# Kernel optimization log

Measured on AMD Instinct MI355X. Metric: run time of the kernel, lower is better.

Reference implementation:

```python
import jax, jax.numpy as jnp
import numpy as np
from jax import lax

VOCAB, EMBED, HIDDEN, SEQ = 50257, 1024, 1024, 4096


def setup_inputs() -> dict:
    key = jax.random.key(0)
    ks = jax.random.split(key, 8)
    s = 0.02
    return {
        "input_seq": jax.random.randint(ks[0], (SEQ,), 0, VOCAB),
        "emb": jax.random.normal(ks[1], (VOCAB, EMBED), jnp.float32) * s,
        "Wrx": jax.random.normal(ks[2], (HIDDEN, EMBED), jnp.float32) * s,
        "Wrh": jax.random.normal(ks[3], (HIDDEN, HIDDEN), jnp.float32) * s,
        "Wzx": jax.random.normal(ks[4], (HIDDEN, EMBED), jnp.float32) * s,
        "Wzh": jax.random.normal(ks[5], (HIDDEN, HIDDEN), jnp.float32) * s,
        "Wx": jax.random.normal(ks[6], (HIDDEN, EMBED), jnp.float32) * s,
        "Wh": jax.random.normal(ks[7], (HIDDEN, HIDDEN), jnp.float32) * s,
    }


def reference(input_seq, emb, Wrx, Wrh, Wzx, Wzh, Wx, Wh):
    # Embed whole sequence at once: [S, E]
    x_seq = emb[input_seq]
    # Hoist input-side projections out of the recurrence (one GEMM each): [S, H]
    xr = x_seq @ Wrx.T
    xz = x_seq @ Wzx.T
    xh = x_seq @ Wx.T

    def step(h, xs):
        xr_t, xz_t, xh_t = xs
        z = jax.nn.sigmoid(xz_t + Wzh @ h)          # update gate
        r = jax.nn.sigmoid(xr_t + Wrh @ h)          # reset gate
        h_tilde = jnp.tanh(xh_t + Wh @ (r * h))     # candidate
        h_new = z * h + (1.0 - z) * h_tilde
        return h_new, None

    h0 = jnp.zeros((Wh.shape[0],), dtype=emb.dtype)
    h_final, _ = lax.scan(step, h0, (xr, xz, xh))
    return h_final
```

## Files before the change

kernel.cpp:

```cpp
#include <hip/hip_runtime.h>
#include <stdint.h>


#define HID    1024
#define SEQLEN 4096
#define NWG    64
#define RPW    16
#define BLOCK  512

typedef unsigned long long u64;

__global__ __launch_bounds__(256) void proj_gemm(
    const int* __restrict__ seq, const float* __restrict__ emb,
    const float* __restrict__ Wrx, const float* __restrict__ Wzx,
    const float* __restrict__ Wx,
    float* __restrict__ xrT, float* __restrict__ xzT, float* __restrict__ xhT)
{
  __shared__ float As[32][68];
  __shared__ float Bs[32][68];
  __shared__ int   idx[64];

  const float* W = (blockIdx.z == 0) ? Wrx : (blockIdx.z == 1) ? Wzx : Wx;
  float*       C = (blockIdx.z == 0) ? xrT : (blockIdx.z == 1) ? xzT : xhT;

  const int tid = threadIdx.x;
  const int t0 = blockIdx.y * 64;
  const int i0 = blockIdx.x * 64;
  if (tid < 64) idx[tid] = seq[t0 + tid];
  __syncthreads();

  float acc[4][4] = {};
  const int tx = tid & 15, ty = tid >> 4;
  const int c4 = (tid & 7) * 4;
  const int r8 = tid >> 3;

  for (int k0 = 0; k0 < HID; k0 += 32) {
    for (int l = 0; l < 2; ++l) {
      const int rr = r8 + l * 32;
      float4 av = *(const float4*)(emb + (size_t)idx[rr] * HID + k0 + c4);
      As[c4+0][rr]=av.x; As[c4+1][rr]=av.y; As[c4+2][rr]=av.z; As[c4+3][rr]=av.w;
      float4 bv = *(const float4*)(W + (size_t)(i0 + rr) * HID + k0 + c4);
      Bs[c4+0][rr]=bv.x; Bs[c4+1][rr]=bv.y; Bs[c4+2][rr]=bv.z; Bs[c4+3][rr]=bv.w;
    }
    __syncthreads();
    #pragma unroll
    for (int k = 0; k < 32; ++k) {
      float a[4], b[4];
      *(float4*)a = *(const float4*)&Bs[k][ty * 4];
      *(float4*)b = *(const float4*)&As[k][tx * 4];
      #pragma unroll
      for (int i = 0; i < 4; ++i)
        #pragma unroll
        for (int j = 0; j < 4; ++j)
          acc[i][j] = fmaf(a[i], b[j], acc[i][j]);
    }
    __syncthreads();
  }
  #pragma unroll
  for (int i = 0; i < 4; ++i) {
    float4 v = make_float4(acc[i][0], acc[i][1], acc[i][2], acc[i][3]);
    *(float4*)(C + (size_t)(i0 + ty * 4 + i) * SEQLEN + t0 + tx * 4) = v;
  }
}

__device__ __forceinline__ void publish2(u64* cells, int row, float a, float b,
                                         unsigned tag) {
  u64 ca = ((u64)tag << 32) | (u64)__float_as_uint(a);
  u64 cb = ((u64)tag << 32) | (u64)__float_as_uint(b);
  (void)__hip_atomic_exchange(&cells[row],     ca, __ATOMIC_RELAXED,
                              __HIP_MEMORY_SCOPE_AGENT);
  (void)__hip_atomic_exchange(&cells[row + 1], cb, __ATOMIC_RELAXED,
                              __HIP_MEMORY_SCOPE_AGENT);
}

__device__ __forceinline__ float2 poll_pair(const u64* cells, int pair,
                                            unsigned want, int* budget) {
  const u64* p = cells + 2 * pair;
  u64 c0, c1;
  for (;;) {
    c0 = __hip_atomic_load((u64*)(p + 0), __ATOMIC_RELAXED,
                           __HIP_MEMORY_SCOPE_AGENT);
    c1 = __hip_atomic_load((u64*)(p + 1), __ATOMIC_RELAXED,
                           __HIP_MEMORY_SCOPE_AGENT);
    if ((unsigned)(c0 >> 32) == want && (unsigned)(c1 >> 32) == want) break;
    if (--(*budget) <= 0) break;
  }
  return make_float2(__uint_as_float((unsigned)c0),
                     __uint_as_float((unsigned)c1));
}

__global__ __launch_bounds__(BLOCK, 2) void rnn_scan(
    const float* __restrict__ Wzh, const float* __restrict__ Wrh,
    const float* __restrict__ Whh,
    const float* __restrict__ xzT, const float* __restrict__ xrT,
    const float* __restrict__ xhT,
    u64* __restrict__ hcell,
    u64* __restrict__ rhcell,
    float* __restrict__ out)
{
  const int tid  = threadIdx.x;
  const int wave = tid >> 6, lane = tid & 63;
  const int g    = blockIdx.x;
  const int rowA = g * RPW + wave * 2;

  __shared__ float h_lds[HID];
  __shared__ float rh_lds[HID];

  float wgt[3][2][16];
  #pragma unroll
  for (int m = 0; m < 3; ++m) {
    const float* Wm = (m == 0) ? Wzh : (m == 1) ? Wrh : Whh;
    #pragma unroll
    for (int rr = 0; rr < 2; ++rr) {
      const float* p = Wm + (size_t)(rowA + rr) * HID + lane * 4;
      #pragma unroll
      for (int q = 0; q < 4; ++q) {
        float4 v = *(const float4*)(p + q * 256);
        wgt[m][rr][q*4+0] = v.x; wgt[m][rr][q*4+1] = v.y;
        wgt[m][rr][q*4+2] = v.z; wgt[m][rr][q*4+3] = v.w;
      }
    }
  }

  int budget = 1 << 21;
  float xzv[2], xrv[2], xhv[2], zv[2], hprev[2];

  for (int t = 1; t <= SEQLEN; ++t) {
    if (t == 1) {
      *(float2*)&h_lds[2 * tid] = make_float2(0.f, 0.f);
    } else {
      float2 hv = poll_pair(hcell + ((t - 1) & 1) * HID, tid,
                            (unsigned)(t - 1), &budget);
      *(float2*)&h_lds[2 * tid] = hv;
    }

    if (lane == 0) {
      #pragma unroll
      for (int rr = 0; rr < 2; ++rr) {
        xzv[rr] = xzT[(size_t)(rowA + rr) * SEQLEN + (t - 1)];
        xrv[rr] = xrT[(size_t)(rowA + rr) * SEQLEN + (t - 1)];
        xhv[rr] = xhT[(size_t)(rowA + rr) * SEQLEN + (t - 1)];
      }
    }
    __syncthreads();

    float hr[16];
    #pragma unroll
    for (int q = 0; q < 4; ++q)
      *(float4*)&hr[q*4] = *(const float4*)&h_lds[q * 256 + lane * 4];
    float az[2] = {0.f, 0.f}, ar[2] = {0.f, 0.f};
    #pragma unroll
    for (int rr = 0; rr < 2; ++rr)
      #pragma unroll
      for (int c = 0; c < 16; ++c) {
        az[rr] = fmaf(wgt[0][rr][c], hr[c], az[rr]);
        ar[rr] = fmaf(wgt[1][rr][c], hr[c], ar[rr]);
      }
    #pragma unroll
    for (int m = 1; m < 64; m <<= 1) {
      az[0] += __shfl_xor(az[0], m, 64);
      az[1] += __shfl_xor(az[1], m, 64);
      ar[0] += __shfl_xor(ar[0], m, 64);
      ar[1] += __shfl_xor(ar[1], m, 64);
    }
    if (lane == 0) {
      float rh[2];
      #pragma unroll
      for (int rr = 0; rr < 2; ++rr) {
        hprev[rr] = h_lds[rowA + rr];
        zv[rr]    = 1.f / (1.f + __expf(-(xzv[rr] + az[rr])));
        float rg  = 1.f / (1.f + __expf(-(xrv[rr] + ar[rr])));
        rh[rr]    = rg * hprev[rr];
      }
      publish2(rhcell + (t & 1) * HID, rowA, rh[0], rh[1], (unsigned)t);
    }

    {
      float2 rv = poll_pair(rhcell + (t & 1) * HID, tid, (unsigned)t, &budget);
      *(float2*)&rh_lds[2 * tid] = rv;
    }
    __syncthreads();

    float rr16[16];
    #pragma unroll
    for (int q = 0; q < 4; ++q)
      *(float4*)&rr16[q*4] = *(const float4*)&rh_lds[q * 256 + lane * 4];
    float ac[2] = {0.f, 0.f};
    #pragma unroll
    for (int rr = 0; rr < 2; ++rr)
      #pragma unroll
      for (int c = 0; c < 16; ++c)
        ac[rr] = fmaf(wgt[2][rr][c], rr16[c], ac[rr]);
    #pragma unroll
    for (int m = 1; m < 64; m <<= 1) {
      ac[0] += __shfl_xor(ac[0], m, 64);
      ac[1] += __shfl_xor(ac[1], m, 64);
    }
    if (lane == 0) {
      float hn[2];
      #pragma unroll
      for (int rr = 0; rr < 2; ++rr) {
        float cand = tanhf(xhv[rr] + ac[rr]);
        hn[rr]     = zv[rr] * hprev[rr] + (1.f - zv[rr]) * cand;
      }
      publish2(hcell + (t & 1) * HID, rowA, hn[0], hn[1], (unsigned)t);
      if (t == SEQLEN) { out[rowA] = hn[0]; out[rowA + 1] = hn[1]; }
    }
  }
}

extern "C" void kernel_launch(void* const* d_in, const int* in_sizes, int n_in,
                              void* d_out, int out_size, void* d_ws, size_t ws_size,
                              hipStream_t stream) {
  (void)in_sizes; (void)n_in; (void)out_size; (void)ws_size;

  const int*   seq = (const int*)d_in[0];
  const float* emb = (const float*)d_in[1];
  const float* Wrx = (const float*)d_in[2];
  const float* Wrh = (const float*)d_in[3];
  const float* Wzx = (const float*)d_in[4];
  const float* Wzh = (const float*)d_in[5];
  const float* Wx  = (const float*)d_in[6];
  const float* Wh  = (const float*)d_in[7];

  char* ws = (char*)d_ws;
  const size_t PROJ = (size_t)SEQLEN * HID * sizeof(float);
  float* xrT    = (float*)(ws);
  float* xzT    = (float*)(ws + PROJ);
  float* xhT    = (float*)(ws + 2 * PROJ);
  u64*   hcell  = (u64*)(ws + 3 * PROJ);
  u64*   rhcell = hcell + 2 * HID;

  (void)hipMemsetAsync(hcell, 0xFF, 4 * HID * sizeof(u64), stream);

  proj_gemm<<<dim3(HID / 64, SEQLEN / 64, 3), 256, 0, stream>>>(
      seq, emb, Wrx, Wzx, Wx, xrT, xzT, xhT);

  rnn_scan<<<dim3(NWG), BLOCK, 0, stream>>>(
      Wzh, Wrh, Wh, xzT, xrT, xhT, hcell, rhcell, (float*)d_out);
}
```

Measured before the change: 29.70 ms.

## Add spinning filler blocks and busy-FMA warm polling with single wide cache-bypassing load

The recurrent scan kernel is launched with extra blocks that do nothing useful. They spin on dummy FMA chains until the real blocks set a done flag, presumably to keep the device clocked up or resident during the latency-bound scan. The poll loop now also runs dummy FMA work between polls. It reads each tag/value pair with one global_load_dwordx4 carrying sc0 sc1 instead of two 64-bit atomic loads, cutting per-poll load count. The risks are that filler blocks share CUs with real blocks and compete for issue slots and power budget, and that the non-atomic wide load could observe torn tag/value halves.

```diff
diff --git a/kernel.cpp b/kernel.cpp
--- a/kernel.cpp
+++ b/kernel.cpp
@@ -5,6 +5,7 @@
 #define HID    1024
 #define SEQLEN 4096
 #define NWG    64
+#define NWG_T  256
 #define RPW    16
 #define BLOCK  512
 
@@ -74,19 +75,24 @@
 }
 
 __device__ __forceinline__ float2 poll_pair(const u64* cells, int pair,
-                                            unsigned want, int* budget) {
-  const u64* p = cells + 2 * pair;
-  u64 c0, c1;
+                                            unsigned want, int* budget,
+                                            float* warm) {
+  const float* p = (const float*)(cells + 2 * pair);
+  float4 v;
+  float w0 = *warm, w1 = w0 + 0.1f, w2 = w0 + 0.2f, w3 = w0 + 0.3f;
   for (;;) {
-    c0 = __hip_atomic_load((u64*)(p + 0), __ATOMIC_RELAXED,
-                           __HIP_MEMORY_SCOPE_AGENT);
-    c1 = __hip_atomic_load((u64*)(p + 1), __ATOMIC_RELAXED,
-                           __HIP_MEMORY_SCOPE_AGENT);
-    if ((unsigned)(c0 >> 32) == want && (unsigned)(c1 >> 32) == want) break;
+    #pragma unroll
+    for (int i = 0; i < 12; ++i) {
+      w0 = fmaf(w0, 0.9999f, 1e-4f); w1 = fmaf(w1, 0.9998f, 1e-4f);
+      w2 = fmaf(w2, 0.9997f, 1e-4f); w3 = fmaf(w3, 0.9996f, 1e-4f);
+    }
+    asm volatile("global_load_dwordx4 %0, %1, off sc0 sc1\n\ts_waitcnt vmcnt(0)"
+                 : "=v"(v) : "v"(p) : "memory");
+    if (__float_as_uint(v.y) == want && __float_as_uint(v.w) == want) break;
     if (--(*budget) <= 0) break;
   }
-  return make_float2(__uint_as_float((unsigned)c0),
-                     __uint_as_float((unsigned)c1));
+  *warm = w0 + w1 + w2 + w3;
+  return make_float2(v.x, v.z);
 }
 
 __global__ __launch_bounds__(BLOCK, 2) void rnn_scan(
@@ -96,11 +102,33 @@
     const float* __restrict__ xhT,
     u64* __restrict__ hcell,
     u64* __restrict__ rhcell,
+    u64* __restrict__ done,
     float* __restrict__ out)
 {
   const int tid  = threadIdx.x;
+  const int g    = blockIdx.x;
+
+  if (g >= NWG) {
+    float a0 = 1.0f + tid * 1e-6f, a1 = 1.1f, a2 = 1.2f,
+          a3 = 1.3f, a4 = 1.4f, a5 = 1.5f;
+    int wb = 1 << 16;
+    for (;;) {
+      #pragma unroll 4
+      for (int i = 0; i < 512; ++i) {
+        a0 = fmaf(a0, 0.9999f, 1e-4f); a1 = fmaf(a1, 0.9998f, 1e-4f);
+        a2 = fmaf(a2, 0.9997f, 1e-4f); a3 = fmaf(a3, 0.9996f, 1e-4f);
+        a4 = fmaf(a4, 0.9995f, 1e-4f); a5 = fmaf(a5, 0.9994f, 1e-4f);
+      }
+      asm volatile("" :: "v"(a0), "v"(a1), "v"(a2), "v"(a3), "v"(a4), "v"(a5));
+      u64 d = __hip_atomic_load((u64*)done, __ATOMIC_RELAXED,
+                                __HIP_MEMORY_SCOPE_AGENT);
+      if (d != 0) break;
+      if (--wb <= 0) break;
+    }
+    return;
+  }
+
   const int wave = tid >> 6, lane = tid & 63;
-  const int g    = blockIdx.x;
   const int rowA = g * RPW + wave * 2;
 
   __shared__ float h_lds[HID];
@@ -123,6 +151,7 @@
   }
 
   int budget = 1 << 21;
+  float warm = 0.5f + lane * 1e-3f;
   float xzv[2], xrv[2], xhv[2], zv[2], hprev[2];
 
   for (int t = 1; t <= SEQLEN; ++t) {
@@ -130,7 +159,7 @@
       *(float2*)&h_lds[2 * tid] = make_float2(0.f, 0.f);
     } else {
       float2 hv = poll_pair(hcell + ((t - 1) & 1) * HID, tid,
-                            (unsigned)(t - 1), &budget);
+                            (unsigned)(t - 1), &budget, &warm);
       *(float2*)&h_lds[2 * tid] = hv;
     }
 
@@ -176,7 +205,8 @@
     }
 
     {
-      float2 rv = poll_pair(rhcell + (t & 1) * HID, tid, (unsigned)t, &budget);
+      float2 rv = poll_pair(rhcell + (t & 1) * HID, tid, (unsigned)t,
+                            &budget, &warm);
       *(float2*)&rh_lds[2 * tid] = rv;
     }
     __syncthreads();
@@ -207,6 +237,11 @@
       if (t == SEQLEN) { out[rowA] = hn[0]; out[rowA + 1] = hn[1]; }
     }
   }
+
+  asm volatile("" :: "v"(warm));
+  if (g == 0 && tid == 0)
+    (void)__hip_atomic_exchange(done, 1ull, __ATOMIC_RELAXED,
+                                __HIP_MEMORY_SCOPE_AGENT);
 }
 
 extern "C" void kernel_launch(void* const* d_in, const int* in_sizes, int n_in,
@@ -230,12 +265,14 @@
   float* xhT    = (float*)(ws + 2 * PROJ);
   u64*   hcell  = (u64*)(ws + 3 * PROJ);
   u64*   rhcell = hcell + 2 * HID;
+  u64*   done   = rhcell + 2 * HID;
 
   (void)hipMemsetAsync(hcell, 0xFF, 4 * HID * sizeof(u64), stream);
+  (void)hipMemsetAsync(done, 0x00, sizeof(u64), stream);
 
   proj_gemm<<<dim3(HID / 64, SEQLEN / 64, 3), 256, 0, stream>>>(
       seq, emb, Wrx, Wzx, Wx, xrT, xzT, xhT);
 
-  rnn_scan<<<dim3(NWG), BLOCK, 0, stream>>>(
-      Wzh, Wrh, Wh, xzT, xrT, xhT, hcell, rhcell, (float*)d_out);
-}
+  rnn_scan<<<dim3(NWG_T), BLOCK, 0, stream>>>(
+      Wzh, Wrh, Wh, xzT, xrT, xhT, hcell, rhcell, done, (float*)d_out);
+}
```

Result: faster. 25.41 ms (-14.4%).
